# Kernel optimization log

Hardware: AMD Instinct MI355X
Metric: run time of the kernel (lower is better)

The kernel has to match this reference:

```python
import jax, jax.numpy as jnp
import numpy as np

HASHMAPS = [(50, 32, 1.0), (200, 16, 0.5), (400, 8, 0.25), (400, 4, 0.125), (400, 3, 0.05)]
CONCAT = 63  # 32+16+8+4+3
PRIMES = jnp.array([73856093, 19349663, 83492791], dtype=jnp.int32)
# corner order idx = i*4 + j*2 + k, bit 0 -> floor, bit 1 -> ceil (matches torch loop)
BITS = jnp.array([[i, j, k] for i in range(2) for j in range(2) for k in range(2)], dtype=jnp.int32)  # (8,3)


def _encode(pos, table, vsl):
    # pos: (N,3) float32; table: (hsize, D)
    p = pos / vsl
    fl = jnp.floor(p)
    fl_i = fl.astype(jnp.int32)
    ce_i = jnp.ceil(p).astype(jnp.int32)
    sel = jnp.where(BITS[None, :, :] == 0, fl_i[:, None, :], ce_i[:, None, :])  # (N,8,3) int32
    sp = sel * PRIMES  # int32 wraparound, same as torch
    h = jnp.mod((sp[..., 0] ^ sp[..., 1]) ^ sp[..., 2], table.shape[0])  # (N,8), nonneg
    emb = table[h]  # (N,8,D) gather
    r = p - fl  # (N,3) trilinear fractions
    # faithful to original: frac weights the FLOOR-corner group (m1/m2/m3 masks)
    lin1 = r[:, 0:1, None] * emb[:, :4] + (1.0 - r[:, 0:1, None]) * emb[:, 4:]   # (N,4,D)
    lin2 = r[:, 1:2, None] * lin1[:, :2] + (1.0 - r[:, 1:2, None]) * lin1[:, 2:]  # (N,2,D)
    lin3 = r[:, 2:3] * lin2[:, 0] + (1.0 - r[:, 2:3]) * lin2[:, 1]               # (N,D)
    return lin3


def setup_inputs() -> dict:
    key = jax.random.key(0)
    ks = jax.random.split(key, 16)
    N = 262144
    inp = {"x": jax.random.normal(ks[0], (N, 3), dtype=jnp.float32)}
    for lvl, (hsize, dim, _) in enumerate(HASHMAPS):
        inp[f"emb{lvl}"] = jax.random.normal(ks[1 + lvl], (hsize, dim), dtype=jnp.float32)
    s = 1.0 / np.sqrt(CONCAT)
    inp["Wd1"] = jax.random.uniform(ks[6], (CONCAT, CONCAT), jnp.float32, -s, s)
    inp["bd1"] = jax.random.uniform(ks[7], (CONCAT,), jnp.float32, -s, s)
    inp["Wd2"] = jax.random.uniform(ks[8], (CONCAT, 1), jnp.float32, -s, s)
    inp["bd2"] = jax.random.uniform(ks[9], (1,), jnp.float32, -s, s)
    inp["Wc1"] = jax.random.uniform(ks[10], (CONCAT, CONCAT), jnp.float32, -s, s)
    inp["bc1"] = jax.random.uniform(ks[11], (CONCAT,), jnp.float32, -s, s)
    inp["Wc2"] = jax.random.uniform(ks[12], (CONCAT, 3), jnp.float32, -s, s)
    inp["bc2"] = jax.random.uniform(ks[13], (3,), jnp.float32, -s, s)
    return inp


def reference(x, emb0, emb1, emb2, emb3, emb4, Wd1, bd1, Wd2, bd2, Wc1, bc1, Wc2, bc2):
    tables = [emb0, emb1, emb2, emb3, emb4]
    feats = [_encode(x, tables[i], HASHMAPS[i][2]) for i in range(5)]
    f = jnp.concatenate(feats, axis=1)  # (N,63)
    dense = jax.nn.relu(f @ Wd1 + bd1) @ Wd2 + bd2  # (N,1)
    color = jax.nn.relu(f @ Wc1 + bc1) @ Wc2 + bc2  # (N,3)
    return (dense, color)
```

## Files before the change

kernel.cpp:

```cpp
#include <hip/hip_runtime.h>
#include <hip/hip_fp16.h>


#define NPTS 262144
#define BLOCK 512
#define PTS_PER_BLOCK 128

#define IMG_TAB   0
#define IMG_WTF   32768
#define IMG_BW    49152
#define IMG_BYTES 51200

#define OFF_L0 0
#define OFF_L1 2000
#define OFF_L2 6000
#define OFF_L3 10800
#define OFF_L4 12400
#define TAB_HALFS 16384

typedef _Float16 f16x8 __attribute__((ext_vector_type(8)));
typedef _Float16 f16x4 __attribute__((ext_vector_type(4)));
typedef float f32x4 __attribute__((ext_vector_type(4)));

__device__ __forceinline__ void async_cp16(const void* g, void* l) {
    __builtin_amdgcn_global_load_lds(
        (__attribute__((address_space(1))) unsigned int*)const_cast<void*>(g),
        (__attribute__((address_space(3))) unsigned int*)l, 16, 0, 0);
}

__global__ void prep_kernel(const float* __restrict__ Wd1, const float* __restrict__ bd1,
                            const float* __restrict__ Wd2,
                            const float* __restrict__ Wc1, const float* __restrict__ bc1,
                            const float* __restrict__ Wc2,
                            const float* __restrict__ e0, const float* __restrict__ e1,
                            const float* __restrict__ e2, const float* __restrict__ e3,
                            const float* __restrict__ e4,
                            void* __restrict__ ws) {
    _Float16* tab = (_Float16*)((char*)ws + IMG_TAB);
    _Float16* wtf = (_Float16*)((char*)ws + IMG_WTF);
    float*    bw  = (float*)((char*)ws + IMG_BW);
    const int gtid = blockIdx.x * blockDim.x + threadIdx.x;
    const int gstr = gridDim.x * blockDim.x;

    for (int i = gtid; i < 1024; i += gstr) {
        int nt = i >> 7, rem = i & 127, s = rem >> 6, l = rem & 63;
        int kq = l >> 4, lo = l & 15, col = nt * 16 + lo;
#pragma unroll
        for (int j = 0; j < 8; ++j) {
            int k = s * 32 + kq * 8 + j;
            float v = 0.f;
            if (k < 63) {
                if (col < 63) v = Wd1[k * 63 + col];
                else if (col >= 64 && col < 127) v = Wc1[k * 63 + (col - 64)];
            }
            wtf[i * 8 + j] = (_Float16)v;
        }
    }
    for (int i = gtid; i < 512; i += gstr) {
        float v = 0.f;
        if (i < 128) {
            if (i < 63) v = bd1[i];
            else if (i >= 64 && i < 127) v = bc1[i - 64];
        } else if (i < 192) {
            int t = i - 128; v = (t < 63) ? Wd2[t] : 0.f;
        } else if (i < 448) {
            int t = i - 192, c = t >> 2, j = t & 3;
            v = (c < 63 && j < 3) ? Wc2[c * 3 + j] : 0.f;
        }
        bw[i] = v;
    }
    for (int idx = gtid; idx < 50 * 40; idx += gstr) {
        int r = idx / 40, c = idx - r * 40;
        tab[OFF_L0 + idx] = (c < 32) ? (_Float16)e0[r * 32 + c] : (_Float16)0.f;
    }
    for (int idx = gtid; idx < 200 * 20; idx += gstr) {
        int r = idx / 20, c = idx - r * 20;
        tab[OFF_L1 + idx] = (c < 16) ? (_Float16)e1[r * 16 + c] : (_Float16)0.f;
    }
    for (int idx = gtid; idx < 400 * 12; idx += gstr) {
        int r = idx / 12, c = idx - r * 12;
        tab[OFF_L2 + idx] = (c < 8) ? (_Float16)e2[r * 8 + c] : (_Float16)0.f;
    }
    for (int idx = gtid; idx < 400 * 4; idx += gstr)
        tab[OFF_L3 + idx] = (_Float16)e3[idx];
    for (int idx = gtid; idx < 400 * 4; idx += gstr) {
        int r = idx >> 2, c = idx & 3;
        tab[OFF_L4 + idx] = (c < 3) ? (_Float16)e4[r * 3 + c] : (_Float16)0.f;
    }
    for (int idx = 14000 + gtid; idx < TAB_HALFS; idx += gstr)
        tab[idx] = (_Float16)0.f;
}

__device__ __forceinline__ int pymod(int v, int H, int sh) {
    unsigned vu = (unsigned)v ^ 0x80000000u;
    unsigned q = __umulhi(vu >> sh, 0x51EB851Fu) >> 3;
    int m = (int)(vu - q * (unsigned)H);
    int h = m - 48;
    return h < 0 ? h + H : h;
}

struct Corner {
    int ax0, ax1, ay0, ay1, az0, az1;
    float rx, ry, rz;
};
__device__ __forceinline__ Corner mkcorner(float px, float py, float pz) {
    Corner c;
    float fx = floorf(px), fy = floorf(py), fz = floorf(pz);
    c.rx = px - fx; c.ry = py - fy; c.rz = pz - fz;
    c.ax0 = (int)((unsigned)(int)fx * 73856093u);
    c.ax1 = (int)((unsigned)(int)ceilf(px) * 73856093u);
    c.ay0 = (int)((unsigned)(int)fy * 19349663u);
    c.ay1 = (int)((unsigned)(int)ceilf(py) * 19349663u);
    c.az0 = (int)((unsigned)(int)fz * 83492791u);
    c.az1 = (int)((unsigned)(int)ceilf(pz) * 83492791u);
    return c;
}

#define CXOR(C, cc) ((((cc) & 4) ? C.ax1 : C.ax0) ^ (((cc) & 2) ? C.ay1 : C.ay0) \
                   ^ (((cc) & 1) ? C.az1 : C.az0))
#define CW(C, cc) ((((cc) & 4) ? (1.f - C.rx) : C.rx) * \
                   (((cc) & 2) ? (1.f - C.ry) : C.ry) * \
                   (((cc) & 1) ? (1.f - C.rz) : C.rz))

__global__ __launch_bounds__(BLOCK, 6) void nerf_fwd(
    const float* __restrict__ x,
    const float* __restrict__ bd2, const float* __restrict__ bc2,
    const void* __restrict__ ws,
    float* __restrict__ out)
{
    __shared__ __align__(16) char ldsb[IMG_BYTES];
    const int tid = threadIdx.x;

    {
        const char* gsrc = (const char*)ws + tid * 16;
        char* ldst = ldsb + tid * 16;
#pragma unroll
        for (int i = 0; i < 6; ++i)
            async_cp16(gsrc + i * 8192, ldst + i * 8192);
        if (tid < 128)
            async_cp16(gsrc + 6 * 8192, ldst + 6 * 8192);
    }

    const int l  = tid & 63;
    const int lo = l & 15;
    const int kq = l >> 4;
    const int wb = blockIdx.x * PTS_PER_BLOCK + (tid >> 6) * 16;
    const int p  = wb + lo;

    const float x0 = x[3 * p + 0], x1 = x[3 * p + 1], x2 = x[3 * p + 2];

    Corner ca = mkcorner(x0, x1, x2);

    const bool q2 = (kq == 2), q3 = (kq == 3);
    const int  g  = kq >> 1;
    const int  H  = 200 << g;
    const int  sh = 3 + g;
    const float sA = q3 ? 8.f : (q2 ? 4.f : 2.f);
    const int tb0 = q3 ? OFF_L3 : (q2 ? OFF_L2 : OFF_L1);
    const int st  = q3 ? 4 : (q2 ? 12 : 20);
    const int fo0 = (kq == 1) ? 8 : 0;

    const float b0x = x0 * sA, b0y = x1 * sA, b0z = x2 * sA;
    Corner cb = mkcorner(b0x, b0y, b0z);

    const float dx = x0 / 0.05f, dy = x1 / 0.05f, dz = x2 / 0.05f;
    const float b1x = q3 ? dx : b0x, b1y = q3 ? dy : b0y, b1z = q3 ? dz : b0z;
    Corner cb1 = mkcorner(b1x, b1y, b1z);
    const int tb1 = q3 ? OFF_L4 : tb0;
    const int fo1 = q3 ? 0 : fo0 + 4;

    int hA[8], h0[8], h1[8];
#pragma unroll
    for (int cc = 0; cc < 8; ++cc) hA[cc] = pymod(CXOR(ca, cc), 50, 1);
#pragma unroll
    for (int cc = 0; cc < 8; ++cc) h0[cc] = pymod(CXOR(cb, cc), H, sh);
#pragma unroll
    for (int cc = 0; cc < 8; ++cc) h1[cc] = pymod(CXOR(cb1, cc), H, sh);

    const float bd2v = bd2[0];
    const float bcx = bc2[0], bcy = bc2[1], bcz = bc2[2];

    __syncthreads();

    const _Float16* ldsT = (const _Float16*)ldsb;

    const int kq8 = kq * 8;
    f16x8 va[8];
#pragma unroll
    for (int cc = 0; cc < 8; ++cc)
        va[cc] = *(const f16x8*)(ldsT + OFF_L0 + hA[cc] * 40 + kq8);
    f16x4 ea[8];
#pragma unroll
    for (int cc = 0; cc < 8; ++cc)
        ea[cc] = *(const f16x4*)(ldsT + tb0 + h0[cc] * st + fo0);

    float fA[8] = {0.f, 0.f, 0.f, 0.f, 0.f, 0.f, 0.f, 0.f};
#pragma unroll
    for (int cc = 0; cc < 8; ++cc) {
        float w = CW(ca, cc);
#pragma unroll
        for (int j = 0; j < 8; ++j)
            fA[j] = fmaf((float)va[cc][j], w, fA[j]);
    }

    f16x4 eb[8];
#pragma unroll
    for (int cc = 0; cc < 8; ++cc)
        eb[cc] = *(const f16x4*)(ldsT + tb1 + h1[cc] * st + fo1);

    float fB[8] = {0.f, 0.f, 0.f, 0.f, 0.f, 0.f, 0.f, 0.f};
#pragma unroll
    for (int cc = 0; cc < 8; ++cc) {
        float w = CW(cb, cc);
        fB[0] = fmaf((float)ea[cc][0], w, fB[0]); fB[1] = fmaf((float)ea[cc][1], w, fB[1]);
        fB[2] = fmaf((float)ea[cc][2], w, fB[2]); fB[3] = fmaf((float)ea[cc][3], w, fB[3]);
    }
#pragma unroll
    for (int cc = 0; cc < 8; ++cc) {
        float w = CW(cb1, cc);
        fB[4] = fmaf((float)eb[cc][0], w, fB[4]); fB[5] = fmaf((float)eb[cc][1], w, fB[5]);
        fB[6] = fmaf((float)eb[cc][2], w, fB[6]); fB[7] = fmaf((float)eb[cc][3], w, fB[7]);
    }
    if (q3) fB[7] = 0.f;

    union AF { unsigned u[4]; f16x8 h; } a0, a1;
#pragma unroll
    for (int j = 0; j < 4; ++j) {
        __half2 t0 = __floats2half2_rn(fA[2 * j], fA[2 * j + 1]);
        __half2 t1 = __floats2half2_rn(fB[2 * j], fB[2 * j + 1]);
        a0.u[j] = *(unsigned*)&t0;
        a1.u[j] = *(unsigned*)&t1;
    }

    const f16x8* wtf = (const f16x8*)(ldsb + IMG_WTF);
    const float* b1c = (const float*)(ldsb + IMG_BW);
    const float* w2d = b1c + 128;
    const float4* w2c = (const float4*)(b1c + 192);

    float pd[4]  = {0.f, 0.f, 0.f, 0.f};
    float pc0[4] = {0.f, 0.f, 0.f, 0.f};
    float pc1[4] = {0.f, 0.f, 0.f, 0.f};
    float pc2[4] = {0.f, 0.f, 0.f, 0.f};

#pragma unroll
    for (int nt = 0; nt < 8; ++nt) {
        f16x8 b0 = wtf[(nt * 2 + 0) * 64 + l];
        f16x8 b1 = wtf[(nt * 2 + 1) * 64 + l];
        f32x4 c = {0.f, 0.f, 0.f, 0.f};
        c = __builtin_amdgcn_mfma_f32_16x16x32_f16(a0.h, b0, c, 0, 0, 0);
        c = __builtin_amdgcn_mfma_f32_16x16x32_f16(a1.h, b1, c, 0, 0, 0);
        float bias = b1c[nt * 16 + lo];
        if (nt < 4) {
            float w2 = w2d[nt * 16 + lo];
#pragma unroll
            for (int r = 0; r < 4; ++r)
                pd[r] = fmaf(fmaxf(c[r] + bias, 0.f), w2, pd[r]);
        } else {
            float4 wc = w2c[(nt - 4) * 16 + lo];
#pragma unroll
            for (int r = 0; r < 4; ++r) {
                float t = fmaxf(c[r] + bias, 0.f);
                pc0[r] = fmaf(t, wc.x, pc0[r]);
                pc1[r] = fmaf(t, wc.y, pc1[r]);
                pc2[r] = fmaf(t, wc.z, pc2[r]);
            }
        }
    }

#pragma unroll
    for (int r = 0; r < 4; ++r) {
        float v = pd[r];
        v += __shfl_xor(v, 1); v += __shfl_xor(v, 2);
        v += __shfl_xor(v, 4); v += __shfl_xor(v, 8);
        pd[r] = v;
        float v0 = pc0[r];
        v0 += __shfl_xor(v0, 1); v0 += __shfl_xor(v0, 2);
        v0 += __shfl_xor(v0, 4); v0 += __shfl_xor(v0, 8);
        pc0[r] = v0;
        float v1 = pc1[r];
        v1 += __shfl_xor(v1, 1); v1 += __shfl_xor(v1, 2);
        v1 += __shfl_xor(v1, 4); v1 += __shfl_xor(v1, 8);
        pc1[r] = v1;
        float v2 = pc2[r];
        v2 += __shfl_xor(v2, 1); v2 += __shfl_xor(v2, 2);
        v2 += __shfl_xor(v2, 4); v2 += __shfl_xor(v2, 8);
        pc2[r] = v2;
    }

    if (lo < 4) {
        float badd = (lo == 0) ? bd2v : ((lo == 1) ? bcx : ((lo == 2) ? bcy : bcz));
#pragma unroll
        for (int r = 0; r < 4; ++r) {
            int row = wb + kq * 4 + r;
            int addr = (lo == 0) ? row : (NPTS + row * 3 + (lo - 1));
            float v = (lo == 0) ? pd[r]
                    : ((lo == 1) ? pc0[r] : ((lo == 2) ? pc1[r] : pc2[r]));
            out[addr] = v + badd;
        }
    }
}

extern "C" void kernel_launch(void* const* d_in, const int* in_sizes, int n_in,
                              void* d_out, int out_size, void* d_ws, size_t ws_size,
                              hipStream_t stream) {
    const float* x   = (const float*)d_in[0];
    const float* e0  = (const float*)d_in[1];
    const float* e1  = (const float*)d_in[2];
    const float* e2  = (const float*)d_in[3];
    const float* e3  = (const float*)d_in[4];
    const float* e4  = (const float*)d_in[5];
    const float* Wd1 = (const float*)d_in[6];
    const float* bd1 = (const float*)d_in[7];
    const float* Wd2 = (const float*)d_in[8];
    const float* bd2 = (const float*)d_in[9];
    const float* Wc1 = (const float*)d_in[10];
    const float* bc1 = (const float*)d_in[11];
    const float* Wc2 = (const float*)d_in[12];
    const float* bc2 = (const float*)d_in[13];
    float* out = (float*)d_out;

    prep_kernel<<<64, 256, 0, stream>>>(Wd1, bd1, Wd2, Wc1, bc1, Wc2,
                                        e0, e1, e2, e3, e4, d_ws);
    nerf_fwd<<<dim3(NPTS / PTS_PER_BLOCK), dim3(BLOCK), 0, stream>>>(
        x, bd2, bc2, d_ws, out);
}
```

Baseline: 36.27 us.

## Process two point tiles per block to amortize LDS staging; use DPP row reductions

Each block now handles two 128-point tiles instead of one, so the roughly 50 KB LDS image of tables and weights is loaded once per two tiles and the grid halves. The second tile's coordinate loads are issued up front, and its hashing is computed after the first tile's body. The cross-lane reductions switch from __shfl_xor to DPP row_ror adds. The trade-off is fewer blocks, less parallelism, and possibly higher register pressure. The launch code must halve its grid size, which is in the unseen part.

```diff
diff --git a/kernel.cpp b/kernel.cpp
--- a/kernel.cpp
+++ b/kernel.cpp
@@ -4,7 +4,9 @@
 
 #define NPTS 262144
 #define BLOCK 512
-#define PTS_PER_BLOCK 128
+#define PTS_PER_TILE 128
+#define TILES 2
+#define PTS_PER_BLOCK (PTS_PER_TILE * TILES)
 
 #define IMG_TAB   0
 #define IMG_WTF   32768
@@ -122,6 +124,115 @@
                    (((cc) & 2) ? (1.f - C.ry) : C.ry) * \
                    (((cc) & 1) ? (1.f - C.rz) : C.rz))
 
+#define ROR_ADD(v, CTRL) { \
+    int _t = __builtin_amdgcn_update_dpp(0, __float_as_int(v), (CTRL), 0xF, 0xF, true); \
+    (v) += __int_as_float(_t); }
+__device__ __forceinline__ float rowsum16(float v) {
+    ROR_ADD(v, 0x121)
+    ROR_ADD(v, 0x122)
+    ROR_ADD(v, 0x124)
+    ROR_ADD(v, 0x128)
+    return v;
+}
+
+#define TILE_BODY(ca_, cb_, cb1_, hA_, h0_, h1_, wb_)                          \
+{                                                                              \
+    const int kq8 = kq * 8;                                                    \
+    f16x8 va[8];                                                               \
+    _Pragma("unroll")                                                          \
+    for (int cc = 0; cc < 8; ++cc)                                             \
+        va[cc] = *(const f16x8*)(ldsT + OFF_L0 + hA_[cc] * 40 + kq8);          \
+    f16x4 ea[8];                                                               \
+    _Pragma("unroll")                                                          \
+    for (int cc = 0; cc < 8; ++cc)                                             \
+        ea[cc] = *(const f16x4*)(ldsT + tb0 + h0_[cc] * st + fo0);             \
+    float fA[8] = {0.f, 0.f, 0.f, 0.f, 0.f, 0.f, 0.f, 0.f};                    \
+    _Pragma("unroll")                                                          \
+    for (int cc = 0; cc < 8; ++cc) {                                           \
+        float w = CW(ca_, cc);                                                 \
+        _Pragma("unroll")                                                      \
+        for (int j = 0; j < 8; ++j)                                            \
+            fA[j] = fmaf((float)va[cc][j], w, fA[j]);                          \
+    }                                                                          \
+    f16x4 eb[8];                                                               \
+    _Pragma("unroll")                                                          \
+    for (int cc = 0; cc < 8; ++cc)                                             \
+        eb[cc] = *(const f16x4*)(ldsT + tb1 + h1_[cc] * st + fo1);             \
+    float fB[8] = {0.f, 0.f, 0.f, 0.f, 0.f, 0.f, 0.f, 0.f};                    \
+    _Pragma("unroll")                                                          \
+    for (int cc = 0; cc < 8; ++cc) {                                           \
+        float w = CW(cb_, cc);                                                 \
+        fB[0] = fmaf((float)ea[cc][0], w, fB[0]);                              \
+        fB[1] = fmaf((float)ea[cc][1], w, fB[1]);                              \
+        fB[2] = fmaf((float)ea[cc][2], w, fB[2]);                              \
+        fB[3] = fmaf((float)ea[cc][3], w, fB[3]);                              \
+    }                                                                          \
+    _Pragma("unroll")                                                          \
+    for (int cc = 0; cc < 8; ++cc) {                                           \
+        float w = CW(cb1_, cc);                                                \
+        fB[4] = fmaf((float)eb[cc][0], w, fB[4]);                              \
+        fB[5] = fmaf((float)eb[cc][1], w, fB[5]);                              \
+        fB[6] = fmaf((float)eb[cc][2], w, fB[6]);                              \
+        fB[7] = fmaf((float)eb[cc][3], w, fB[7]);                              \
+    }                                                                          \
+    if (q3) fB[7] = 0.f;                                                       \
+    union AF { unsigned u[4]; f16x8 h; } a0, a1;                               \
+    _Pragma("unroll")                                                          \
+    for (int j = 0; j < 4; ++j) {                                              \
+        __half2 t0 = __floats2half2_rn(fA[2 * j], fA[2 * j + 1]);              \
+        __half2 t1 = __floats2half2_rn(fB[2 * j], fB[2 * j + 1]);              \
+        a0.u[j] = *(unsigned*)&t0;                                             \
+        a1.u[j] = *(unsigned*)&t1;                                             \
+    }                                                                          \
+    float pd[4]  = {0.f, 0.f, 0.f, 0.f};                                       \
+    float pc0[4] = {0.f, 0.f, 0.f, 0.f};                                       \
+    float pc1[4] = {0.f, 0.f, 0.f, 0.f};                                       \
+    float pc2[4] = {0.f, 0.f, 0.f, 0.f};                                       \
+    _Pragma("unroll")                                                          \
+    for (int nt = 0; nt < 8; ++nt) {                                           \
+        f16x8 b0 = wtf[(nt * 2 + 0) * 64 + l];                                 \
+        f16x8 b1 = wtf[(nt * 2 + 1) * 64 + l];                                 \
+        f32x4 c = {0.f, 0.f, 0.f, 0.f};                                        \
+        c = __builtin_amdgcn_mfma_f32_16x16x32_f16(a0.h, b0, c, 0, 0, 0);      \
+        c = __builtin_amdgcn_mfma_f32_16x16x32_f16(a1.h, b1, c, 0, 0, 0);      \
+        float bias = b1c[nt * 16 + lo];                                        \
+        if (nt < 4) {                                                          \
+            float w2 = w2d[nt * 16 + lo];                                      \
+            _Pragma("unroll")                                                  \
+            for (int r = 0; r < 4; ++r)                                        \
+                pd[r] = fmaf(fmaxf(c[r] + bias, 0.f), w2, pd[r]);              \
+        } else {                                                               \
+            float4 wc = w2c[(nt - 4) * 16 + lo];                               \
+            _Pragma("unroll")                                                  \
+            for (int r = 0; r < 4; ++r) {                                      \
+                float t = fmaxf(c[r] + bias, 0.f);                             \
+                pc0[r] = fmaf(t, wc.x, pc0[r]);                                \
+                pc1[r] = fmaf(t, wc.y, pc1[r]);                                \
+                pc2[r] = fmaf(t, wc.z, pc2[r]);                                \
+            }                                                                  \
+        }                                                                      \
+    }                                                                          \
+    _Pragma("unroll")                                                          \
+    for (int r = 0; r < 4; ++r) {                                              \
+        pd[r]  = rowsum16(pd[r]);                                              \
+        pc0[r] = rowsum16(pc0[r]);                                             \
+        pc1[r] = rowsum16(pc1[r]);                                             \
+        pc2[r] = rowsum16(pc2[r]);                                             \
+    }                                                                          \
+    if (lo < 4) {                                                              \
+        float badd = (lo == 0) ? bd2v                                          \
+                   : ((lo == 1) ? bcx : ((lo == 2) ? bcy : bcz));              \
+        _Pragma("unroll")                                                      \
+        for (int r = 0; r < 4; ++r) {                                          \
+            int row = wb_ + kq * 4 + r;                                        \
+            int addr = (lo == 0) ? row : (NPTS + row * 3 + (lo - 1));          \
+            float v = (lo == 0) ? pd[r]                                        \
+                    : ((lo == 1) ? pc0[r] : ((lo == 2) ? pc1[r] : pc2[r]));    \
+            out[addr] = v + badd;                                              \
+        }                                                                      \
+    }                                                                          \
+}
+
 __global__ __launch_bounds__(BLOCK, 6) void nerf_fwd(
     const float* __restrict__ x,
     const float* __restrict__ bd2, const float* __restrict__ bc2,
@@ -144,12 +255,12 @@
     const int l  = tid & 63;
     const int lo = l & 15;
     const int kq = l >> 4;
-    const int wb = blockIdx.x * PTS_PER_BLOCK + (tid >> 6) * 16;
-    const int p  = wb + lo;
-
-    const float x0 = x[3 * p + 0], x1 = x[3 * p + 1], x2 = x[3 * p + 2];
-
-    Corner ca = mkcorner(x0, x1, x2);
+    const int wb0 = blockIdx.x * PTS_PER_BLOCK + (tid >> 6) * 16;
+    const int wb1 = wb0 + PTS_PER_TILE;
+
+    const int p0 = wb0 + lo, p1 = wb1 + lo;
+    const float x00 = x[3 * p0 + 0], x01 = x[3 * p0 + 1], x02 = x[3 * p0 + 2];
+    const float x10 = x[3 * p1 + 0], x11 = x[3 * p1 + 1], x12 = x[3 * p1 + 2];
 
     const bool q2 = (kq == 2), q3 = (kq == 3);
     const int  g  = kq >> 1;
@@ -159,23 +270,25 @@
     const int tb0 = q3 ? OFF_L3 : (q2 ? OFF_L2 : OFF_L1);
     const int st  = q3 ? 4 : (q2 ? 12 : 20);
     const int fo0 = (kq == 1) ? 8 : 0;
-
-    const float b0x = x0 * sA, b0y = x1 * sA, b0z = x2 * sA;
-    Corner cb = mkcorner(b0x, b0y, b0z);
-
-    const float dx = x0 / 0.05f, dy = x1 / 0.05f, dz = x2 / 0.05f;
-    const float b1x = q3 ? dx : b0x, b1y = q3 ? dy : b0y, b1z = q3 ? dz : b0z;
-    Corner cb1 = mkcorner(b1x, b1y, b1z);
     const int tb1 = q3 ? OFF_L4 : tb0;
     const int fo1 = q3 ? 0 : fo0 + 4;
 
-    int hA[8], h0[8], h1[8];
-#pragma unroll
-    for (int cc = 0; cc < 8; ++cc) hA[cc] = pymod(CXOR(ca, cc), 50, 1);
-#pragma unroll
-    for (int cc = 0; cc < 8; ++cc) h0[cc] = pymod(CXOR(cb, cc), H, sh);
-#pragma unroll
-    for (int cc = 0; cc < 8; ++cc) h1[cc] = pymod(CXOR(cb1, cc), H, sh);
+    Corner ca0 = mkcorner(x00, x01, x02);
+    Corner cb0 = mkcorner(x00 * sA, x01 * sA, x02 * sA);
+    Corner cc0;
+    {
+        const float dx = x00 / 0.05f, dy = x01 / 0.05f, dz = x02 / 0.05f;
+        const float b1x = q3 ? dx : x00 * sA, b1y = q3 ? dy : x01 * sA,
+                    b1z = q3 ? dz : x02 * sA;
+        cc0 = mkcorner(b1x, b1y, b1z);
+    }
+    int hA0[8], h00[8], h10[8];
+#pragma unroll
+    for (int cc = 0; cc < 8; ++cc) hA0[cc] = pymod(CXOR(ca0, cc), 50, 1);
+#pragma unroll
+    for (int cc = 0; cc < 8; ++cc) h00[cc] = pymod(CXOR(cb0, cc), H, sh);
+#pragma unroll
+    for (int cc = 0; cc < 8; ++cc) h10[cc] = pymod(CXOR(cc0, cc), H, sh);
 
     const float bd2v = bd2[0];
     const float bcx = bc2[0], bcy = bc2[1], bcz = bc2[2];
@@ -183,121 +296,31 @@
     __syncthreads();
 
     const _Float16* ldsT = (const _Float16*)ldsb;
-
-    const int kq8 = kq * 8;
-    f16x8 va[8];
-#pragma unroll
-    for (int cc = 0; cc < 8; ++cc)
-        va[cc] = *(const f16x8*)(ldsT + OFF_L0 + hA[cc] * 40 + kq8);
-    f16x4 ea[8];
-#pragma unroll
-    for (int cc = 0; cc < 8; ++cc)
-        ea[cc] = *(const f16x4*)(ldsT + tb0 + h0[cc] * st + fo0);
-
-    float fA[8] = {0.f, 0.f, 0.f, 0.f, 0.f, 0.f, 0.f, 0.f};
-#pragma unroll
-    for (int cc = 0; cc < 8; ++cc) {
-        float w = CW(ca, cc);
-#pragma unroll
-        for (int j = 0; j < 8; ++j)
-            fA[j] = fmaf((float)va[cc][j], w, fA[j]);
-    }
-
-    f16x4 eb[8];
-#pragma unroll
-    for (int cc = 0; cc < 8; ++cc)
-        eb[cc] = *(const f16x4*)(ldsT + tb1 + h1[cc] * st + fo1);
-
-    float fB[8] = {0.f, 0.f, 0.f, 0.f, 0.f, 0.f, 0.f, 0.f};
-#pragma unroll
-    for (int cc = 0; cc < 8; ++cc) {
-        float w = CW(cb, cc);
-        fB[0] = fmaf((float)ea[cc][0], w, fB[0]); fB[1] = fmaf((float)ea[cc][1], w, fB[1]);
-        fB[2] = fmaf((float)ea[cc][2], w, fB[2]); fB[3] = fmaf((float)ea[cc][3], w, fB[3]);
-    }
-#pragma unroll
-    for (int cc = 0; cc < 8; ++cc) {
-        float w = CW(cb1, cc);
-        fB[4] = fmaf((float)eb[cc][0], w, fB[4]); fB[5] = fmaf((float)eb[cc][1], w, fB[5]);
-        fB[6] = fmaf((float)eb[cc][2], w, fB[6]); fB[7] = fmaf((float)eb[cc][3], w, fB[7]);
-    }
-    if (q3) fB[7] = 0.f;
-
-    union AF { unsigned u[4]; f16x8 h; } a0, a1;
-#pragma unroll
-    for (int j = 0; j < 4; ++j) {
-        __half2 t0 = __floats2half2_rn(fA[2 * j], fA[2 * j + 1]);
-        __half2 t1 = __floats2half2_rn(fB[2 * j], fB[2 * j + 1]);
-        a0.u[j] = *(unsigned*)&t0;
-        a1.u[j] = *(unsigned*)&t1;
-    }
-
     const f16x8* wtf = (const f16x8*)(ldsb + IMG_WTF);
     const float* b1c = (const float*)(ldsb + IMG_BW);
     const float* w2d = b1c + 128;
     const float4* w2c = (const float4*)(b1c + 192);
 
-    float pd[4]  = {0.f, 0.f, 0.f, 0.f};
-    float pc0[4] = {0.f, 0.f, 0.f, 0.f};
-    float pc1[4] = {0.f, 0.f, 0.f, 0.f};
-    float pc2[4] = {0.f, 0.f, 0.f, 0.f};
-
-#pragma unroll
-    for (int nt = 0; nt < 8; ++nt) {
-        f16x8 b0 = wtf[(nt * 2 + 0) * 64 + l];
-        f16x8 b1 = wtf[(nt * 2 + 1) * 64 + l];
-        f32x4 c = {0.f, 0.f, 0.f, 0.f};
-        c = __builtin_amdgcn_mfma_f32_16x16x32_f16(a0.h, b0, c, 0, 0, 0);
-        c = __builtin_amdgcn_mfma_f32_16x16x32_f16(a1.h, b1, c, 0, 0, 0);
-        float bias = b1c[nt * 16 + lo];
-        if (nt < 4) {
-            float w2 = w2d[nt * 16 + lo];
-#pragma unroll
-            for (int r = 0; r < 4; ++r)
-                pd[r] = fmaf(fmaxf(c[r] + bias, 0.f), w2, pd[r]);
-        } else {
-            float4 wc = w2c[(nt - 4) * 16 + lo];
-#pragma unroll
-            for (int r = 0; r < 4; ++r) {
-                float t = fmaxf(c[r] + bias, 0.f);
-                pc0[r] = fmaf(t, wc.x, pc0[r]);
-                pc1[r] = fmaf(t, wc.y, pc1[r]);
-                pc2[r] = fmaf(t, wc.z, pc2[r]);
-            }
-        }
-    }
-
-#pragma unroll
-    for (int r = 0; r < 4; ++r) {
-        float v = pd[r];
-        v += __shfl_xor(v, 1); v += __shfl_xor(v, 2);
-        v += __shfl_xor(v, 4); v += __shfl_xor(v, 8);
-        pd[r] = v;
-        float v0 = pc0[r];
-        v0 += __shfl_xor(v0, 1); v0 += __shfl_xor(v0, 2);
-        v0 += __shfl_xor(v0, 4); v0 += __shfl_xor(v0, 8);
-        pc0[r] = v0;
-        float v1 = pc1[r];
-        v1 += __shfl_xor(v1, 1); v1 += __shfl_xor(v1, 2);
-        v1 += __shfl_xor(v1, 4); v1 += __shfl_xor(v1, 8);
-        pc1[r] = v1;
-        float v2 = pc2[r];
-        v2 += __shfl_xor(v2, 1); v2 += __shfl_xor(v2, 2);
-        v2 += __shfl_xor(v2, 4); v2 += __shfl_xor(v2, 8);
-        pc2[r] = v2;
-    }
-
-    if (lo < 4) {
-        float badd = (lo == 0) ? bd2v : ((lo == 1) ? bcx : ((lo == 2) ? bcy : bcz));
-#pragma unroll
-        for (int r = 0; r < 4; ++r) {
-            int row = wb + kq * 4 + r;
-            int addr = (lo == 0) ? row : (NPTS + row * 3 + (lo - 1));
-            float v = (lo == 0) ? pd[r]
-                    : ((lo == 1) ? pc0[r] : ((lo == 2) ? pc1[r] : pc2[r]));
-            out[addr] = v + badd;
-        }
-    }
+    TILE_BODY(ca0, cb0, cc0, hA0, h00, h10, wb0)
+
+    Corner ca1 = mkcorner(x10, x11, x12);
+    Corner cb1 = mkcorner(x10 * sA, x11 * sA, x12 * sA);
+    Corner cc1;
+    {
+        const float dx = x10 / 0.05f, dy = x11 / 0.05f, dz = x12 / 0.05f;
+        const float b1x = q3 ? dx : x10 * sA, b1y = q3 ? dy : x11 * sA,
+                    b1z = q3 ? dz : x12 * sA;
+        cc1 = mkcorner(b1x, b1y, b1z);
+    }
+    int hA1[8], h01[8], h11[8];
+#pragma unroll
+    for (int cc = 0; cc < 8; ++cc) hA1[cc] = pymod(CXOR(ca1, cc), 50, 1);
+#pragma unroll
+    for (int cc = 0; cc < 8; ++cc) h01[cc] = pymod(CXOR(cb1, cc), H, sh);
+#pragma unroll
+    for (int cc = 0; cc < 8; ++cc) h11[cc] = pymod(CXOR(cc1, cc), H, sh);
+
+    TILE_BODY(ca1, cb1, cc1, hA1, h01, h11, wb1)
 }
 
 extern "C" void kernel_launch(void* const* d_in, const int* in_sizes, int n_in,
```

Measured after the change: 36.13 us. Within noise of the previous version (-0.4%).

## Double block size and use DPP row-rotate reductions instead of shuffles

Applied to the files above, without the earlier changes.

Doubles the block to 1024 threads and 256 points, so each block's LDS image of tables and weights is loaded once for twice as many points, which halves the per-point staging traffic and the number of block launches. The async copy loop is rescaled to match. The 16-lane xor-shuffle reductions are replaced with DPP row_ror adds, which avoid the LDS-routed shuffle path. Launch bounds rise to 8, which can raise register pressure, and larger blocks wait longer at the barrier. Fewer, larger blocks may also balance worse across CUs.

```diff
diff --git a/kernel.cpp b/kernel.cpp
--- a/kernel.cpp
+++ b/kernel.cpp
@@ -3,8 +3,8 @@
 
 
 #define NPTS 262144
-#define BLOCK 512
-#define PTS_PER_BLOCK 128
+#define BLOCK 1024
+#define PTS_PER_BLOCK 256
 
 #define IMG_TAB   0
 #define IMG_WTF   32768
@@ -122,7 +122,18 @@
                    (((cc) & 2) ? (1.f - C.ry) : C.ry) * \
                    (((cc) & 1) ? (1.f - C.rz) : C.rz))
 
-__global__ __launch_bounds__(BLOCK, 6) void nerf_fwd(
+#define ROR_ADD(v, CTRL) { \
+    int _t = __builtin_amdgcn_update_dpp(0, __float_as_int(v), (CTRL), 0xF, 0xF, true); \
+    (v) += __int_as_float(_t); }
+__device__ __forceinline__ float rowsum16(float v) {
+    ROR_ADD(v, 0x121)
+    ROR_ADD(v, 0x122)
+    ROR_ADD(v, 0x124)
+    ROR_ADD(v, 0x128)
+    return v;
+}
+
+__global__ __launch_bounds__(BLOCK, 8) void nerf_fwd(
     const float* __restrict__ x,
     const float* __restrict__ bd2, const float* __restrict__ bc2,
     const void* __restrict__ ws,
@@ -135,10 +146,10 @@
         const char* gsrc = (const char*)ws + tid * 16;
         char* ldst = ldsb + tid * 16;
 #pragma unroll
-        for (int i = 0; i < 6; ++i)
-            async_cp16(gsrc + i * 8192, ldst + i * 8192);
+        for (int i = 0; i < 3; ++i)
+            async_cp16(gsrc + i * 16384, ldst + i * 16384);
         if (tid < 128)
-            async_cp16(gsrc + 6 * 8192, ldst + 6 * 8192);
+            async_cp16(gsrc + 3 * 16384, ldst + 3 * 16384);
     }
 
     const int l  = tid & 63;
@@ -148,8 +159,6 @@
     const int p  = wb + lo;
 
     const float x0 = x[3 * p + 0], x1 = x[3 * p + 1], x2 = x[3 * p + 2];
-
-    Corner ca = mkcorner(x0, x1, x2);
 
     const bool q2 = (kq == 2), q3 = (kq == 3);
     const int  g  = kq >> 1;
@@ -159,16 +168,18 @@
     const int tb0 = q3 ? OFF_L3 : (q2 ? OFF_L2 : OFF_L1);
     const int st  = q3 ? 4 : (q2 ? 12 : 20);
     const int fo0 = (kq == 1) ? 8 : 0;
-
-    const float b0x = x0 * sA, b0y = x1 * sA, b0z = x2 * sA;
-    Corner cb = mkcorner(b0x, b0y, b0z);
-
-    const float dx = x0 / 0.05f, dy = x1 / 0.05f, dz = x2 / 0.05f;
-    const float b1x = q3 ? dx : b0x, b1y = q3 ? dy : b0y, b1z = q3 ? dz : b0z;
-    Corner cb1 = mkcorner(b1x, b1y, b1z);
     const int tb1 = q3 ? OFF_L4 : tb0;
     const int fo1 = q3 ? 0 : fo0 + 4;
 
+    Corner ca = mkcorner(x0, x1, x2);
+    Corner cb = mkcorner(x0 * sA, x1 * sA, x2 * sA);
+    Corner cb1;
+    {
+        const float dx = x0 / 0.05f, dy = x1 / 0.05f, dz = x2 / 0.05f;
+        const float b1x = q3 ? dx : x0 * sA, b1y = q3 ? dy : x1 * sA,
+                    b1z = q3 ? dz : x2 * sA;
+        cb1 = mkcorner(b1x, b1y, b1z);
+    }
     int hA[8], h0[8], h1[8];
 #pragma unroll
     for (int cc = 0; cc < 8; ++cc) hA[cc] = pymod(CXOR(ca, cc), 50, 1);
@@ -183,6 +194,10 @@
     __syncthreads();
 
     const _Float16* ldsT = (const _Float16*)ldsb;
+    const f16x8* wtf = (const f16x8*)(ldsb + IMG_WTF);
+    const float* b1c = (const float*)(ldsb + IMG_BW);
+    const float* w2d = b1c + 128;
+    const float4* w2c = (const float4*)(b1c + 192);
 
     const int kq8 = kq * 8;
     f16x8 va[8];
@@ -231,11 +246,6 @@
         a0.u[j] = *(unsigned*)&t0;
         a1.u[j] = *(unsigned*)&t1;
     }
-
-    const f16x8* wtf = (const f16x8*)(ldsb + IMG_WTF);
-    const float* b1c = (const float*)(ldsb + IMG_BW);
-    const float* w2d = b1c + 128;
-    const float4* w2c = (const float4*)(b1c + 192);
 
     float pd[4]  = {0.f, 0.f, 0.f, 0.f};
     float pc0[4] = {0.f, 0.f, 0.f, 0.f};
@@ -269,22 +279,10 @@
 
 #pragma unroll
     for (int r = 0; r < 4; ++r) {
-        float v = pd[r];
-        v += __shfl_xor(v, 1); v += __shfl_xor(v, 2);
-        v += __shfl_xor(v, 4); v += __shfl_xor(v, 8);
-        pd[r] = v;
-        float v0 = pc0[r];
-        v0 += __shfl_xor(v0, 1); v0 += __shfl_xor(v0, 2);
-        v0 += __shfl_xor(v0, 4); v0 += __shfl_xor(v0, 8);
-        pc0[r] = v0;
-        float v1 = pc1[r];
-        v1 += __shfl_xor(v1, 1); v1 += __shfl_xor(v1, 2);
-        v1 += __shfl_xor(v1, 4); v1 += __shfl_xor(v1, 8);
-        pc1[r] = v1;
-        float v2 = pc2[r];
-        v2 += __shfl_xor(v2, 1); v2 += __shfl_xor(v2, 2);
-        v2 += __shfl_xor(v2, 4); v2 += __shfl_xor(v2, 8);
-        pc2[r] = v2;
+        pd[r]  = rowsum16(pd[r]);
+        pc0[r] = rowsum16(pc0[r]);
+        pc1[r] = rowsum16(pc1[r]);
+        pc2[r] = rowsum16(pc2[r]);
     }
 
     if (lo < 4) {
```

Measured after the change: 38.00 us. 4.8% more time.
